# Performance work log

Measured on AMD Instinct MI355X. Metric: run time of the kernel, lower is better.

Reference implementation:

```python
import jax, jax.numpy as jnp
import numpy as np

N, K = 16384, 32          # num bboxes, context size
IN_F, HID = 608, 384      # in_features, hidden_dim
ALPHA = 0.2               # LeakyReLU slope
NEG_INF = -9e15


def setup_inputs() -> dict:
    key = jax.random.key(0)
    k1, k2, k3, k4, k5, k6, k7, k8 = jax.random.split(key, 8)
    h_i = jax.random.normal(k1, (N, IN_F), dtype=jnp.float32)
    idx = jax.random.randint(k2, (N, K), 0, N)
    pad = jax.random.uniform(k3, (N, K)) < 0.2
    context_indices = jnp.where(pad, -1, idx).astype(jnp.int64)
    s_in = 1.0 / np.sqrt(IN_F)
    s_a = 1.0 / np.sqrt(2 * HID)
    W_i = jax.random.uniform(k4, (IN_F, HID), minval=-s_in, maxval=s_in, dtype=jnp.float32)
    W_j = jax.random.uniform(k5, (IN_F, HID), minval=-s_in, maxval=s_in, dtype=jnp.float32)
    a_i = jax.random.uniform(k6, (HID,), minval=-s_a, maxval=s_a, dtype=jnp.float32)
    a_j = jax.random.uniform(k7, (HID,), minval=-s_a, maxval=s_a, dtype=jnp.float32)
    a_b = jax.random.uniform(k8, (1,), minval=-s_a, maxval=s_a, dtype=jnp.float32)
    return {"h_i": h_i, "context_indices": context_indices,
            "W_i": W_i, "W_j": W_j, "a_i": a_i, "a_j": a_j, "a_b": a_b}


def reference(h_i, context_indices, W_i, W_j, a_i, a_j, a_b):
    n = h_i.shape[0]
    Wh_i = h_i @ W_i                          # [N, H]
    # W_j has no bias, so projecting then gathering (zero pad row) equals
    # gathering zero-padded features then projecting.
    Wh_all = h_i @ W_j                        # [N, H]
    Wh_pad = jnp.concatenate([Wh_all, jnp.zeros((1, HID), Wh_all.dtype)], axis=0)
    idx = jnp.where(context_indices >= 0, context_indices, n)   # -1 -> zero row
    Wh_j = Wh_pad[idx]                        # [N, K, H] gather
    # attention_layer(concat(Wh_i, Wh_j)) == Wh_i@a_i + Wh_j@a_j + b
    scores = (Wh_i @ a_i)[:, None] + Wh_j @ a_j + a_b[0]        # [N, K]
    scores = jnp.where(scores > 0, scores, ALPHA * scores)      # LeakyReLU
    scores = jnp.where(context_indices >= 0, scores, NEG_INF)   # mask padding
    att = jax.nn.softmax(scores, axis=1)                        # [N, K]
    h_prime = jnp.einsum('nk,nkh->nh', att, Wh_j)               # [N, H]
    return h_prime
```

## Files before the change

### kernel.cpp

```cpp
#include <hip/hip_runtime.h>
#include <hip/hip_bf16.h>

typedef unsigned short u16;
typedef unsigned int u32;
typedef __attribute__((ext_vector_type(8))) __bf16 bf16x8;
typedef __attribute__((ext_vector_type(4))) __bf16 bf16x4;
typedef __attribute__((ext_vector_type(4))) float f32x4;

#define KCTX 32
#define INF_ 608
#define HID_ 384
#define NBOX 16384

#define AW_OFF  0
#define CNT_OFF 4194304
#define WH_OFF  19922944
#define BT_OFF  32505856
#define V_OFF   32972800
#define SI_OFF  32975232
#define SJ_OFF  33040768
#define AJF_OFF 33106304
#define ABF_OFF 33107840

__device__ __forceinline__ float bfu(u16 u)  { return __uint_as_float(((u32)u) << 16); }
__device__ __forceinline__ float bflo(u32 u) { return __uint_as_float(u << 16); }
__device__ __forceinline__ float bfhi(u32 u) { return __uint_as_float(u & 0xffff0000u); }
__device__ __forceinline__ u16 f2bf(float x) {
  u32 u = __float_as_uint(x);
  return (u16)((u + 0x7fffu + ((u >> 16) & 1u)) >> 16);
}
__device__ __forceinline__ void async_ld16(const void* g, void* l) {
  __builtin_amdgcn_global_load_lds(
      (const __attribute__((address_space(1))) u32*)g,
      (__attribute__((address_space(3))) u32*)l, 16, 0, 0);
}

__device__ __forceinline__ int detect_f32(const u32* hw) {
  const u32 w = hw[threadIdx.x & 63];
  const int e = (int)((w >> 7) & 0xffu);
  const unsigned long long mb = __ballot(e > 134 || e < 100);
  return __popcll(mb) >= 16;
}
__device__ __forceinline__ int detect_i64(const int* ci) {
  const int hi = ci[2 * (threadIdx.x & 63) + 1];
  const unsigned long long mz = __ballot(hi == 0 || hi == -1);
  return __popcll(mz) >= 48;
}

__global__ __launch_bounds__(256) void prep_kernel(
    const void* __restrict__ h, const void* __restrict__ Wi,
    const void* __restrict__ Wj, const void* __restrict__ ai,
    const void* __restrict__ aj, const void* __restrict__ ab,
    u16* __restrict__ Bt, float* __restrict__ v,
    float* __restrict__ ajf, float* __restrict__ abf) {
  __shared__ u16 tile[64][65];
  const int f32m = detect_f32((const u32*)h);
  const int bid = blockIdx.x, tid = threadIdx.x;
  if (bid < 60) {
    const int ft = bid / 6, ht = bid - ft * 6;
    const int f0 = ft * 64, h0 = ht * 64;
    const int ln = tid & 63, fg = tid >> 6;
#pragma unroll
    for (int rr = 0; rr < 16; ++rr) {
      const int fl = fg * 16 + rr;
      const int f = f0 + fl;
      if (f < INF_)
        tile[fl][ln] = f32m ? f2bf(((const float*)Wj)[(size_t)f * HID_ + h0 + ln])
                            : ((const u16*)Wj)[(size_t)f * HID_ + h0 + ln];
    }
    __syncthreads();
#pragma unroll
    for (int rr = 0; rr < 16; ++rr) {
      const int hl = fg * 16 + rr;
      const int f = f0 + ln;
      if (f < INF_) Bt[(size_t)(h0 + hl) * INF_ + f] = tile[ln][hl];
    }
  } else if (bid < 98) {
    const int t = (bid - 60) * 16 + (tid >> 4);
    const int sl = tid & 15;
    if (t < INF_) {
      float s = 0.f;
      if (f32m) {
        const float4* wi = (const float4*)((const float*)Wi + (size_t)t * HID_);
        const float4* a4 = (const float4*)ai;
        for (int c = sl; c < 96; c += 16) {
          float4 x = wi[c], y = a4[c];
          s += x.x * y.x + x.y * y.y + x.z * y.z + x.w * y.w;
        }
      } else {
        const uint4* wi = (const uint4*)((const u16*)Wi + (size_t)t * HID_);
        const uint4* a4 = (const uint4*)ai;
        for (int c = sl; c < 48; c += 16) {
          uint4 x = wi[c], y = a4[c];
          s += bflo(x.x) * bflo(y.x) + bfhi(x.x) * bfhi(y.x)
             + bflo(x.y) * bflo(y.y) + bfhi(x.y) * bfhi(y.y)
             + bflo(x.z) * bflo(y.z) + bfhi(x.z) * bfhi(y.z)
             + bflo(x.w) * bflo(y.w) + bfhi(x.w) * bfhi(y.w);
        }
      }
      s += __shfl_xor(s, 1); s += __shfl_xor(s, 2);
      s += __shfl_xor(s, 4); s += __shfl_xor(s, 8);
      if (sl == 0) v[t] = s;
    }
  } else {
    for (int j = tid; j < HID_; j += 256)
      ajf[j] = f32m ? ((const float*)aj)[j] : bfu(((const u16*)aj)[j]);
    if (tid == 0)
      abf[0] = f32m ? ((const float*)ab)[0] : bfu(((const u16*)ab)[0]);
  }
}

#define ASRO 612
__global__ __launch_bounds__(512, 2) void gemm_fused(
    const void* __restrict__ A, const u16* __restrict__ Bt,
    const float* __restrict__ v, u16* __restrict__ C,
    float* __restrict__ si, const float* __restrict__ ajf,
    float* __restrict__ sj) {
  extern __shared__ __align__(16) char smem[];
  u16* As = (u16*)smem;
  u16* Bs = (u16*)(smem + 78336);
  const int f32m = detect_f32((const u32*)A);
  const int tid  = threadIdx.x;
  const int lane = tid & 63;
  const int wv   = tid >> 6;
  const int row0 = blockIdx.x * 64;
  const char* Btb = (const char*)Bt;

#pragma unroll
  for (int i = 0; i < 3; ++i) {
    const int c = tid + i * 512;
    async_ld16(Btb + (size_t)(c >> 2) * 1216 + (c & 3) * 16, (char*)Bs + c * 16);
  }

  {
    const int g = tid >> 3, sub = tid & 7;
    float s = 0.f;
    const float4* v4 = (const float4*)v;
    if (f32m) {
      const float4* hr = (const float4*)((const float*)A + (size_t)(row0 + g) * INF_);
#pragma unroll
      for (int k = 0; k < 19; ++k) {
        const int c4 = sub + 8 * k;
        float4 x = hr[c4];
        ushort4 sv;
        sv.x = f2bf(x.x); sv.y = f2bf(x.y); sv.z = f2bf(x.z); sv.w = f2bf(x.w);
        *(ushort4*)&As[g * ASRO + c4 * 4] = sv;
        float4 w = v4[c4];
        s += x.x * w.x + x.y * w.y + x.z * w.z + x.w * w.w;
      }
    } else {
      const uint4* hr = (const uint4*)((const u16*)A + (size_t)(row0 + g) * INF_);
      for (int k = 0; k < 10; ++k) {
        const int c8 = sub + 8 * k;
        if (c8 < 76) {
          uint4 x = hr[c8];
          *(ushort4*)&As[g * ASRO + c8 * 8]     = *(ushort4*)&x.x;
          *(ushort4*)&As[g * ASRO + c8 * 8 + 4] = *(ushort4*)&x.z;
          float4 w0 = v4[2 * c8], w1 = v4[2 * c8 + 1];
          s += bflo(x.x) * w0.x + bfhi(x.x) * w0.y + bflo(x.y) * w0.z + bfhi(x.y) * w0.w
             + bflo(x.z) * w1.x + bfhi(x.z) * w1.y + bflo(x.w) * w1.z + bfhi(x.w) * w1.w;
        }
      }
    }
    s += __shfl_xor(s, 1); s += __shfl_xor(s, 2); s += __shfl_xor(s, 4);
    if (sub == 0) si[row0 + g] = s;
  }

  f32x4 acc[4][3];
#pragma unroll
  for (int i = 0; i < 4; ++i)
#pragma unroll
    for (int j = 0; j < 3; ++j) acc[i][j] = (f32x4){0.f, 0.f, 0.f, 0.f};

  const int lm = lane & 15, q = lane >> 4;
  const int n0 = wv * 48;

  __syncthreads();
  int cur = 0;
  for (int kt = 0; kt < 19; ++kt) {
    if (kt < 18) {
      const size_t kb = (size_t)(kt + 1) * 64;
#pragma unroll
      for (int i = 0; i < 3; ++i) {
        const int c = tid + i * 512;
        async_ld16(Btb + (size_t)(c >> 2) * 1216 + kb + (c & 3) * 16,
                   (char*)Bs + (cur ^ 1) * 24576 + c * 16);
      }
    }
    bf16x8 af[4], bfr[3];
#pragma unroll
    for (int im = 0; im < 4; ++im) {
      const int r = im * 16 + lm;
      bf16x4 lo = *(const bf16x4*)&As[r * ASRO + kt * 32 + q * 8];
      bf16x4 hi = *(const bf16x4*)&As[r * ASRO + kt * 32 + q * 8 + 4];
      af[im] = __builtin_shufflevector(lo, hi, 0, 1, 2, 3, 4, 5, 6, 7);
    }
#pragma unroll
    for (int in = 0; in < 3; ++in)
      bfr[in] = *(const bf16x8*)&Bs[cur * 12288 + (n0 + in * 16 + lm) * 32 + q * 8];
#pragma unroll
    for (int im = 0; im < 4; ++im)
#pragma unroll
      for (int in = 0; in < 3; ++in)
        acc[im][in] = __builtin_amdgcn_mfma_f32_16x16x32_bf16(
            af[im], bfr[in], acc[im][in], 0, 0, 0);
    __syncthreads();
    cur ^= 1;
  }

#pragma unroll
  for (int im = 0; im < 4; ++im)
#pragma unroll
    for (int in = 0; in < 3; ++in) {
      const int cw = in * 16 + lm;
#pragma unroll
      for (int r = 0; r < 4; ++r) {
        const int rowg = row0 + im * 16 + q * 4 + r;
        C[((size_t)wv * NBOX + rowg) * 48 + cw] = f2bf(acc[im][in][r]);
      }
    }
  float* sjred = (float*)Bs;
  float ajv[3];
#pragma unroll
  for (int in = 0; in < 3; ++in) ajv[in] = ajf[n0 + in * 16 + lm];
#pragma unroll
  for (int im = 0; im < 4; ++im)
#pragma unroll
    for (int r = 0; r < 4; ++r) {
      float p = acc[im][0][r] * ajv[0] + acc[im][1][r] * ajv[1]
              + acc[im][2][r] * ajv[2];
      p += __shfl_xor(p, 1); p += __shfl_xor(p, 2);
      p += __shfl_xor(p, 4); p += __shfl_xor(p, 8);
      if (lm == 0) sjred[wv * 64 + im * 16 + q * 4 + r] = p;
    }
  __syncthreads();
  if (tid < 64) {
    float s = 0.f;
#pragma unroll
    for (int w = 0; w < 8; ++w) s += sjred[w * 64 + tid];
    sj[row0 + tid] = s;
  }
}

__global__ __launch_bounds__(256) void score_kernel(
    const int* __restrict__ ci, const float* __restrict__ si,
    const float* __restrict__ sj, const float* __restrict__ abf,
    float2* __restrict__ aw, int* __restrict__ cnt) {
  const int i64 = detect_i64(ci);
  const int tid = threadIdx.x;
  const int k = tid & 31;
  const int n = blockIdx.x * 8 + (tid >> 5);
  const size_t t = (size_t)n * KCTX + k;
  int idx;
  if (i64) { int lo = ci[2 * t], hi2 = ci[2 * t + 1]; idx = (hi2 < 0) ? -1 : lo; }
  else     { idx = ci[t]; }
  const bool valid = idx >= 0;
  const float sjv = valid ? sj[idx] : 0.f;
  float raw = si[n] + sjv + abf[0];
  float lr = raw > 0.f ? raw : 0.2f * raw;
  float s = valid ? lr : -9e15f;
  float m = s;
#pragma unroll
  for (int o = 16; o; o >>= 1) m = fmaxf(m, __shfl_xor(m, o, 32));
  float p = __expf(s - m);
  float d = p;
#pragma unroll
  for (int o = 16; o; o >>= 1) d += __shfl_xor(d, o, 32);
  const float w = p / d;
  const unsigned long long bm = __ballot(valid);
  const u32 m32 = (u32)(bm >> (tid & 32));
  const int c_ = __popc(m32);
  const int r4 = (c_ + 3) & ~3;
  if (valid) {
    const int pf = __popc(m32 & ((1u << k) - 1u));
    aw[(size_t)n * KCTX + pf] = (float2){w, __int_as_float(idx)};
  }
  if (k >= c_ && k < r4) aw[(size_t)n * KCTX + k] = (float2){0.f, 0.f};
  if (k == 0) cnt[n] = r4;
}

__global__ __launch_bounds__(384) void gather_kernel(
    const void* __restrict__ h, const float2* __restrict__ aw,
    const int* __restrict__ cnt, const u16* __restrict__ Wh2,
    void* __restrict__ out) {
  __shared__ float2 aws[64 * 33];
  __shared__ int cs[64];
  const int f32m = detect_f32((const u32*)h);
  const int tid = threadIdx.x;
  const int s  = blockIdx.x & 7;
  const int g0 = (blockIdx.x >> 3) * 64;
  const float2* awg = aw + (size_t)g0 * KCTX;
  for (int i = tid; i < 2048; i += 384) aws[(i >> 5) * 33 + (i & 31)] = awg[i];
  if (tid < 64) cs[tid] = cnt[g0 + tid];
  __syncthreads();

  const int r = tid / 6, c = tid - r * 6;
  const int n = g0 + r;
  const u16* bc = Wh2 + (size_t)s * NBOX * 48 + c * 8;
  const int kc = cs[r];
  float a0 = 0, a1 = 0, a2 = 0, a3 = 0, a4 = 0, a5 = 0, a6 = 0, a7 = 0;
  for (int k = 0; k < kc; k += 4) {
    uint4 q[4]; float w4[4];
#pragma unroll
    for (int u = 0; u < 4; ++u) {
      const float2 e = aws[r * 33 + k + u];
      w4[u] = e.x;
      q[u] = *(const uint4*)(bc + (size_t)((u32)__float_as_int(e.y)) * 48);
    }
#pragma unroll
    for (int u = 0; u < 4; ++u) {
      const float w = w4[u];
      a0 += w * bflo(q[u].x); a1 += w * bfhi(q[u].x);
      a2 += w * bflo(q[u].y); a3 += w * bfhi(q[u].y);
      a4 += w * bflo(q[u].z); a5 += w * bfhi(q[u].z);
      a6 += w * bflo(q[u].w); a7 += w * bfhi(q[u].w);
    }
  }
  if (f32m) {
    float4* o4 = (float4*)((float*)out + (size_t)n * HID_ + s * 48 + c * 8);
    o4[0] = (float4){a0, a1, a2, a3};
    o4[1] = (float4){a4, a5, a6, a7};
  } else {
    uint4 o;
    o.x = (u32)f2bf(a0) | ((u32)f2bf(a1) << 16);
    o.y = (u32)f2bf(a2) | ((u32)f2bf(a3) << 16);
    o.z = (u32)f2bf(a4) | ((u32)f2bf(a5) << 16);
    o.w = (u32)f2bf(a6) | ((u32)f2bf(a7) << 16);
    *(uint4*)((u16*)out + (size_t)n * HID_ + s * 48 + c * 8) = o;
  }
}

extern "C" void kernel_launch(void* const* d_in, const int* in_sizes, int n_in,
                              void* d_out, int out_size, void* d_ws, size_t ws_size,
                              hipStream_t stream) {
  const void* h  = d_in[0];
  const int*  ci = (const int*)d_in[1];
  const void* Wi = d_in[2];
  const void* Wj = d_in[3];
  const void* ai = d_in[4];
  const void* aj = d_in[5];
  const void* ab = d_in[6];

  char* ws = (char*)d_ws;
  float2* aw  = (float2*)(ws + AW_OFF);
  int*    cnt = (int*)(ws + CNT_OFF);
  u16*   Wh  = (u16*)(ws + WH_OFF);
  u16*   Bt  = (u16*)(ws + BT_OFF);
  float* v   = (float*)(ws + V_OFF);
  float* si  = (float*)(ws + SI_OFF);
  float* sj  = (float*)(ws + SJ_OFF);
  float* ajf = (float*)(ws + AJF_OFF);
  float* abf = (float*)(ws + ABF_OFF);

  prep_kernel<<<99, 256, 0, stream>>>(h, Wi, Wj, ai, aj, ab, Bt, v, ajf, abf);
  gemm_fused<<<256, 512, 127488, stream>>>(h, Bt, v, Wh, si, ajf, sj);
  score_kernel<<<2048, 256, 0, stream>>>(ci, si, sj, abf, aw, cnt);
  gather_kernel<<<2048, 384, 0, stream>>>(h, aw, cnt, Wh, d_out);
}
```

Before: 161.0 us.

## Replace LDS-staged GEMM with direct-from-global 16-row tiles and more blocks

```diff
diff --git a/kernel.cpp b/kernel.cpp
--- a/kernel.cpp
+++ b/kernel.cpp
@@ -4,7 +4,6 @@
 typedef unsigned short u16;
 typedef unsigned int u32;
 typedef __attribute__((ext_vector_type(8))) __bf16 bf16x8;
-typedef __attribute__((ext_vector_type(4))) __bf16 bf16x4;
 typedef __attribute__((ext_vector_type(4))) float f32x4;
 
 #define KCTX 32
@@ -28,11 +27,6 @@
 __device__ __forceinline__ u16 f2bf(float x) {
   u32 u = __float_as_uint(x);
   return (u16)((u + 0x7fffu + ((u >> 16) & 1u)) >> 16);
-}
-__device__ __forceinline__ void async_ld16(const void* g, void* l) {
-  __builtin_amdgcn_global_load_lds(
-      (const __attribute__((address_space(1))) u32*)g,
-      (__attribute__((address_space(3))) u32*)l, 16, 0, 0);
 }
 
 __device__ __forceinline__ int detect_f32(const u32* hw) {
@@ -110,136 +104,96 @@
   }
 }
 
-#define ASRO 612
-__global__ __launch_bounds__(512, 2) void gemm_fused(
+__global__ __launch_bounds__(256, 4) void gemm_fused(
     const void* __restrict__ A, const u16* __restrict__ Bt,
     const float* __restrict__ v, u16* __restrict__ C,
     float* __restrict__ si, const float* __restrict__ ajf,
     float* __restrict__ sj) {
-  extern __shared__ __align__(16) char smem[];
-  u16* As = (u16*)smem;
-  u16* Bs = (u16*)(smem + 78336);
+  __shared__ float sjred[4][16];
   const int f32m = detect_f32((const u32*)A);
   const int tid  = threadIdx.x;
   const int lane = tid & 63;
   const int wv   = tid >> 6;
-  const int row0 = blockIdx.x * 64;
-  const char* Btb = (const char*)Bt;
-
-#pragma unroll
-  for (int i = 0; i < 3; ++i) {
-    const int c = tid + i * 512;
-    async_ld16(Btb + (size_t)(c >> 2) * 1216 + (c & 3) * 16, (char*)Bs + c * 16);
-  }
-
-  {
-    const int g = tid >> 3, sub = tid & 7;
-    float s = 0.f;
-    const float4* v4 = (const float4*)v;
-    if (f32m) {
-      const float4* hr = (const float4*)((const float*)A + (size_t)(row0 + g) * INF_);
-#pragma unroll
-      for (int k = 0; k < 19; ++k) {
-        const int c4 = sub + 8 * k;
-        float4 x = hr[c4];
-        ushort4 sv;
-        sv.x = f2bf(x.x); sv.y = f2bf(x.y); sv.z = f2bf(x.z); sv.w = f2bf(x.w);
-        *(ushort4*)&As[g * ASRO + c4 * 4] = sv;
-        float4 w = v4[c4];
-        s += x.x * w.x + x.y * w.y + x.z * w.z + x.w * w.w;
+  const int lm   = lane & 15;
+  const int q    = lane >> 4;
+  const int row0 = blockIdx.x * 16;
+  const int n0   = wv * 96;
+
+  const float4* v4 = (const float4*)v;
+  const float* hf = (const float*)A + (size_t)(row0 + lm) * INF_;
+  const u16*   hb = (const u16*)A   + (size_t)(row0 + lm) * INF_;
+
+  const u16* bbase = Bt + (size_t)(n0 + lm) * INF_ + q * 8;
+
+  f32x4 acc[6];
+#pragma unroll
+  for (int j = 0; j < 6; ++j) acc[j] = (f32x4){0.f, 0.f, 0.f, 0.f};
+  float sacc = 0.f;
+
+  for (int kt = 0; kt < 19; ++kt) {
+    const int k0 = kt * 32 + q * 8;
+    bf16x8 af;
+    {
+      const int c4 = k0 >> 2;
+      const float4 w0 = v4[c4], w1 = v4[c4 + 1];
+      if (f32m) {
+        const float4 x0 = *(const float4*)(hf + k0);
+        const float4 x1 = *(const float4*)(hf + k0 + 4);
+        uint4 pk;
+        pk.x = (u32)f2bf(x0.x) | ((u32)f2bf(x0.y) << 16);
+        pk.y = (u32)f2bf(x0.z) | ((u32)f2bf(x0.w) << 16);
+        pk.z = (u32)f2bf(x1.x) | ((u32)f2bf(x1.y) << 16);
+        pk.w = (u32)f2bf(x1.z) | ((u32)f2bf(x1.w) << 16);
+        af = __builtin_bit_cast(bf16x8, pk);
+        sacc += x0.x * w0.x + x0.y * w0.y + x0.z * w0.z + x0.w * w0.w
+              + x1.x * w1.x + x1.y * w1.y + x1.z * w1.z + x1.w * w1.w;
+      } else {
+        const uint4 xb = *(const uint4*)(hb + k0);
+        af = __builtin_bit_cast(bf16x8, xb);
+        sacc += bflo(xb.x) * w0.x + bfhi(xb.x) * w0.y
+              + bflo(xb.y) * w0.z + bfhi(xb.y) * w0.w
+              + bflo(xb.z) * w1.x + bfhi(xb.z) * w1.y
+              + bflo(xb.w) * w1.z + bfhi(xb.w) * w1.w;
       }
-    } else {
-      const uint4* hr = (const uint4*)((const u16*)A + (size_t)(row0 + g) * INF_);
-      for (int k = 0; k < 10; ++k) {
-        const int c8 = sub + 8 * k;
-        if (c8 < 76) {
-          uint4 x = hr[c8];
-          *(ushort4*)&As[g * ASRO + c8 * 8]     = *(ushort4*)&x.x;
-          *(ushort4*)&As[g * ASRO + c8 * 8 + 4] = *(ushort4*)&x.z;
-          float4 w0 = v4[2 * c8], w1 = v4[2 * c8 + 1];
-          s += bflo(x.x) * w0.x + bfhi(x.x) * w0.y + bflo(x.y) * w0.z + bfhi(x.y) * w0.w
-             + bflo(x.z) * w1.x + bfhi(x.z) * w1.y + bflo(x.w) * w1.z + bfhi(x.w) * w1.w;
-        }
-      }
-    }
-    s += __shfl_xor(s, 1); s += __shfl_xor(s, 2); s += __shfl_xor(s, 4);
-    if (sub == 0) si[row0 + g] = s;
-  }
-
-  f32x4 acc[4][3];
-#pragma unroll
-  for (int i = 0; i < 4; ++i)
-#pragma unroll
-    for (int j = 0; j < 3; ++j) acc[i][j] = (f32x4){0.f, 0.f, 0.f, 0.f};
-
-  const int lm = lane & 15, q = lane >> 4;
-  const int n0 = wv * 48;
-
+    }
+    bf16x8 bfr[6];
+#pragma unroll
+    for (int in = 0; in < 6; ++in)
+      bfr[in] = *(const bf16x8*)(bbase + (size_t)in * 16 * INF_ + kt * 32);
+#pragma unroll
+    for (int in = 0; in < 6; ++in)
+      acc[in] = __builtin_amdgcn_mfma_f32_16x16x32_bf16(af, bfr[in], acc[in], 0, 0, 0);
+  }
+
+  sacc += __shfl_xor(sacc, 16);
+  sacc += __shfl_xor(sacc, 32);
+  if (wv == 0 && lane < 16) si[row0 + lane] = sacc;
+
+#pragma unroll
+  for (int in = 0; in < 6; ++in) {
+    const int col = n0 + in * 16 + lm;
+    const int s = col / 48, cw = col - s * 48;
+#pragma unroll
+    for (int r = 0; r < 4; ++r) {
+      const int rowg = row0 + q * 4 + r;
+      C[((size_t)s * NBOX + rowg) * 48 + cw] = f2bf(acc[in][r]);
+    }
+  }
+
+  float ajv[6];
+#pragma unroll
+  for (int in = 0; in < 6; ++in) ajv[in] = ajf[n0 + in * 16 + lm];
+#pragma unroll
+  for (int r = 0; r < 4; ++r) {
+    float p = acc[0][r] * ajv[0] + acc[1][r] * ajv[1] + acc[2][r] * ajv[2]
+            + acc[3][r] * ajv[3] + acc[4][r] * ajv[4] + acc[5][r] * ajv[5];
+    p += __shfl_xor(p, 1); p += __shfl_xor(p, 2);
+    p += __shfl_xor(p, 4); p += __shfl_xor(p, 8);
+    if (lm == 0) sjred[wv][q * 4 + r] = p;
+  }
   __syncthreads();
-  int cur = 0;
-  for (int kt = 0; kt < 19; ++kt) {
-    if (kt < 18) {
-      const size_t kb = (size_t)(kt + 1) * 64;
-#pragma unroll
-      for (int i = 0; i < 3; ++i) {
-        const int c = tid + i * 512;
-        async_ld16(Btb + (size_t)(c >> 2) * 1216 + kb + (c & 3) * 16,
-                   (char*)Bs + (cur ^ 1) * 24576 + c * 16);
-      }
-    }
-    bf16x8 af[4], bfr[3];
-#pragma unroll
-    for (int im = 0; im < 4; ++im) {
-      const int r = im * 16 + lm;
-      bf16x4 lo = *(const bf16x4*)&As[r * ASRO + kt * 32 + q * 8];
-      bf16x4 hi = *(const bf16x4*)&As[r * ASRO + kt * 32 + q * 8 + 4];
-      af[im] = __builtin_shufflevector(lo, hi, 0, 1, 2, 3, 4, 5, 6, 7);
-    }
-#pragma unroll
-    for (int in = 0; in < 3; ++in)
-      bfr[in] = *(const bf16x8*)&Bs[cur * 12288 + (n0 + in * 16 + lm) * 32 + q * 8];
-#pragma unroll
-    for (int im = 0; im < 4; ++im)
-#pragma unroll
-      for (int in = 0; in < 3; ++in)
-        acc[im][in] = __builtin_amdgcn_mfma_f32_16x16x32_bf16(
-            af[im], bfr[in], acc[im][in], 0, 0, 0);
-    __syncthreads();
-    cur ^= 1;
-  }
-
-#pragma unroll
-  for (int im = 0; im < 4; ++im)
-#pragma unroll
-    for (int in = 0; in < 3; ++in) {
-      const int cw = in * 16 + lm;
-#pragma unroll
-      for (int r = 0; r < 4; ++r) {
-        const int rowg = row0 + im * 16 + q * 4 + r;
-        C[((size_t)wv * NBOX + rowg) * 48 + cw] = f2bf(acc[im][in][r]);
-      }
-    }
-  float* sjred = (float*)Bs;
-  float ajv[3];
-#pragma unroll
-  for (int in = 0; in < 3; ++in) ajv[in] = ajf[n0 + in * 16 + lm];
-#pragma unroll
-  for (int im = 0; im < 4; ++im)
-#pragma unroll
-    for (int r = 0; r < 4; ++r) {
-      float p = acc[im][0][r] * ajv[0] + acc[im][1][r] * ajv[1]
-              + acc[im][2][r] * ajv[2];
-      p += __shfl_xor(p, 1); p += __shfl_xor(p, 2);
-      p += __shfl_xor(p, 4); p += __shfl_xor(p, 8);
-      if (lm == 0) sjred[wv * 64 + im * 16 + q * 4 + r] = p;
-    }
-  __syncthreads();
-  if (tid < 64) {
-    float s = 0.f;
-#pragma unroll
-    for (int w = 0; w < 8; ++w) s += sjred[w * 64 + tid];
-    sj[row0 + tid] = s;
-  }
+  if (tid < 16)
+    sj[row0 + tid] = sjred[0][tid] + sjred[1][tid] + sjred[2][tid] + sjred[3][tid];
 }
 
 __global__ __launch_bounds__(256) void score_kernel(
@@ -353,7 +307,7 @@
   float* abf = (float*)(ws + ABF_OFF);
 
   prep_kernel<<<99, 256, 0, stream>>>(h, Wi, Wj, ai, aj, ab, Bt, v, ajf, abf);
-  gemm_fused<<<256, 512, 127488, stream>>>(h, Bt, v, Wh, si, ajf, sj);
+  gemm_fused<<<1024, 256, 0, stream>>>(h, Bt, v, Wh, si, ajf, sj);
   score_kernel<<<2048, 256, 0, stream>>>(ci, si, sj, abf, aw, cnt);
   gather_kernel<<<2048, 384, 0, stream>>>(h, aw, cnt, Wh, d_out);
 }
```

Result: slower. 187.8 us (+16.6%).

## Split bf16 conversion into separate kernel and retile GEMM with per-wave async pipelines

Applied to the files above, without the earlier changes.

```diff
diff --git a/kernel.cpp b/kernel.cpp
--- a/kernel.cpp
+++ b/kernel.cpp
@@ -4,7 +4,6 @@
 typedef unsigned short u16;
 typedef unsigned int u32;
 typedef __attribute__((ext_vector_type(8))) __bf16 bf16x8;
-typedef __attribute__((ext_vector_type(4))) __bf16 bf16x4;
 typedef __attribute__((ext_vector_type(4))) float f32x4;
 
 #define KCTX 32
@@ -21,6 +20,7 @@
 #define SJ_OFF  33040768
 #define AJF_OFF 33106304
 #define ABF_OFF 33107840
+#define HBF_OFF 33554432
 
 __device__ __forceinline__ float bfu(u16 u)  { return __uint_as_float(((u32)u) << 16); }
 __device__ __forceinline__ float bflo(u32 u) { return __uint_as_float(u << 16); }
@@ -51,7 +51,7 @@
     const void* __restrict__ h, const void* __restrict__ Wi,
     const void* __restrict__ Wj, const void* __restrict__ ai,
     const void* __restrict__ aj, const void* __restrict__ ab,
-    u16* __restrict__ Bt, float* __restrict__ v,
+    u16* __restrict__ Bt, float* __restrict__ v, float* __restrict__ sj,
     float* __restrict__ ajf, float* __restrict__ abf) {
   __shared__ u16 tile[64][65];
   const int f32m = detect_f32((const u32*)h);
@@ -103,6 +103,7 @@
       if (sl == 0) v[t] = s;
     }
   } else {
+    for (int j = tid; j < NBOX; j += 256) sj[j] = 0.f;
     for (int j = tid; j < HID_; j += 256)
       ajf[j] = f32m ? ((const float*)aj)[j] : bfu(((const u16*)aj)[j]);
     if (tid == 0)
@@ -110,135 +111,135 @@
   }
 }
 
-#define ASRO 612
-__global__ __launch_bounds__(512, 2) void gemm_fused(
-    const void* __restrict__ A, const u16* __restrict__ Bt,
-    const float* __restrict__ v, u16* __restrict__ C,
-    float* __restrict__ si, const float* __restrict__ ajf,
-    float* __restrict__ sj) {
+__global__ __launch_bounds__(256) void convert_kernel(
+    const void* __restrict__ h, const float* __restrict__ v,
+    u16* __restrict__ hbf, float* __restrict__ si) {
+  const int f32m = detect_f32((const u32*)h);
+  const int g = threadIdx.x >> 3, sub = threadIdx.x & 7;
+  const int row = blockIdx.x * 32 + g;
+  float s = 0.f;
+  const float4* v4 = (const float4*)v;
+  if (f32m) {
+    const float4* hr = (const float4*)((const float*)h + (size_t)row * INF_);
+    u32* ob = (u32*)(hbf + (size_t)row * INF_);
+#pragma unroll
+    for (int k = 0; k < 19; ++k) {
+      const int c4 = sub + 8 * k;
+      float4 x = hr[c4];
+      uint2 pk;
+      pk.x = (u32)f2bf(x.x) | ((u32)f2bf(x.y) << 16);
+      pk.y = (u32)f2bf(x.z) | ((u32)f2bf(x.w) << 16);
+      *(uint2*)&ob[c4 * 2] = pk;
+      float4 w = v4[c4];
+      s += x.x * w.x + x.y * w.y + x.z * w.z + x.w * w.w;
+    }
+  } else {
+    const uint4* hr = (const uint4*)((const u16*)h + (size_t)row * INF_);
+    for (int k = 0; k < 10; ++k) {
+      const int c8 = sub + 8 * k;
+      if (c8 < 76) {
+        uint4 x = hr[c8];
+        float4 w0 = v4[2 * c8], w1 = v4[2 * c8 + 1];
+        s += bflo(x.x) * w0.x + bfhi(x.x) * w0.y + bflo(x.y) * w0.z + bfhi(x.y) * w0.w
+           + bflo(x.z) * w1.x + bfhi(x.z) * w1.y + bflo(x.w) * w1.z + bfhi(x.w) * w1.w;
+      }
+    }
+  }
+  s += __shfl_xor(s, 1); s += __shfl_xor(s, 2); s += __shfl_xor(s, 4);
+  if (sub == 0) si[row] = s;
+}
+
+__global__ __launch_bounds__(256) void gemm_fused(
+    const void* __restrict__ A, const u16* __restrict__ hbf_,
+    const u16* __restrict__ Bt, u16* __restrict__ C,
+    const float* __restrict__ ajf, float* __restrict__ sj) {
   extern __shared__ __align__(16) char smem[];
-  u16* As = (u16*)smem;
-  u16* Bs = (u16*)(smem + 78336);
   const int f32m = detect_f32((const u32*)A);
   const int tid  = threadIdx.x;
   const int lane = tid & 63;
   const int wv   = tid >> 6;
-  const int row0 = blockIdx.x * 64;
-  const char* Btb = (const char*)Bt;
-
-#pragma unroll
-  for (int i = 0; i < 3; ++i) {
-    const int c = tid + i * 512;
-    async_ld16(Btb + (size_t)(c >> 2) * 1216 + (c & 3) * 16, (char*)Bs + c * 16);
-  }
-
-  {
-    const int g = tid >> 3, sub = tid & 7;
-    float s = 0.f;
-    const float4* v4 = (const float4*)v;
-    if (f32m) {
-      const float4* hr = (const float4*)((const float*)A + (size_t)(row0 + g) * INF_);
-#pragma unroll
-      for (int k = 0; k < 19; ++k) {
-        const int c4 = sub + 8 * k;
-        float4 x = hr[c4];
-        ushort4 sv;
-        sv.x = f2bf(x.x); sv.y = f2bf(x.y); sv.z = f2bf(x.z); sv.w = f2bf(x.w);
-        *(ushort4*)&As[g * ASRO + c4 * 4] = sv;
-        float4 w = v4[c4];
-        s += x.x * w.x + x.y * w.y + x.z * w.z + x.w * w.w;
-      }
-    } else {
-      const uint4* hr = (const uint4*)((const u16*)A + (size_t)(row0 + g) * INF_);
-      for (int k = 0; k < 10; ++k) {
-        const int c8 = sub + 8 * k;
-        if (c8 < 76) {
-          uint4 x = hr[c8];
-          *(ushort4*)&As[g * ASRO + c8 * 8]     = *(ushort4*)&x.x;
-          *(ushort4*)&As[g * ASRO + c8 * 8 + 4] = *(ushort4*)&x.z;
-          float4 w0 = v4[2 * c8], w1 = v4[2 * c8 + 1];
-          s += bflo(x.x) * w0.x + bfhi(x.x) * w0.y + bflo(x.y) * w0.z + bfhi(x.y) * w0.w
-             + bflo(x.z) * w1.x + bfhi(x.z) * w1.y + bflo(x.w) * w1.z + bfhi(x.w) * w1.w;
-        }
-      }
-    }
-    s += __shfl_xor(s, 1); s += __shfl_xor(s, 2); s += __shfl_xor(s, 4);
-    if (sub == 0) si[row0 + g] = s;
-  }
-
-  f32x4 acc[4][3];
+  const int lm   = lane & 15, q = lane >> 4;
+  const int panel = blockIdx.x >> 6;
+  const int rowc  = blockIdx.x & 63;
+  const int row0 = rowc * 256 + wv * 64;
+  const int c0   = panel * 96;
+  const char* hB = f32m ? (const char*)hbf_ : (const char*)A;
+  const char* hrow = hB + (size_t)(row0 + (lane >> 2)) * 1216 + (lane & 3) * 16;
+  const char* brow = (const char*)Bt + (size_t)(c0 + (lane >> 2)) * 1216 + (lane & 3) * 16;
+  char* wbase = smem + wv * 20480;
+
+  f32x4 acc[4][6];
+#pragma unroll
+  for (int mf = 0; mf < 4; ++mf)
+#pragma unroll
+    for (int nf = 0; nf < 6; ++nf) acc[mf][nf] = (f32x4){0.f, 0.f, 0.f, 0.f};
+
 #pragma unroll
   for (int i = 0; i < 4; ++i)
-#pragma unroll
-    for (int j = 0; j < 3; ++j) acc[i][j] = (f32x4){0.f, 0.f, 0.f, 0.f};
-
-  const int lm = lane & 15, q = lane >> 4;
-  const int n0 = wv * 48;
-
-  __syncthreads();
+    async_ld16(hrow + i * 19456, wbase + i * 1024 + lane * 16);
+#pragma unroll
+  for (int i = 0; i < 6; ++i)
+    async_ld16(brow + i * 19456, wbase + 4096 + i * 1024 + lane * 16);
+
   int cur = 0;
   for (int kt = 0; kt < 19; ++kt) {
     if (kt < 18) {
-      const size_t kb = (size_t)(kt + 1) * 64;
-#pragma unroll
-      for (int i = 0; i < 3; ++i) {
-        const int c = tid + i * 512;
-        async_ld16(Btb + (size_t)(c >> 2) * 1216 + kb + (c & 3) * 16,
-                   (char*)Bs + (cur ^ 1) * 24576 + c * 16);
+      const int kb = (kt + 1) * 64;
+      char* nb = wbase + (cur ^ 1) * 10240;
+#pragma unroll
+      for (int i = 0; i < 4; ++i)
+        async_ld16(hrow + i * 19456 + kb, nb + i * 1024 + lane * 16);
+#pragma unroll
+      for (int i = 0; i < 6; ++i)
+        async_ld16(brow + i * 19456 + kb, nb + 4096 + i * 1024 + lane * 16);
+      asm volatile("s_waitcnt vmcnt(10)" ::: "memory");
+    } else {
+      asm volatile("s_waitcnt vmcnt(0)" ::: "memory");
+    }
+    __builtin_amdgcn_sched_barrier(0);
+    const char* ab = wbase + cur * 10240;
+    const char* bb = ab + 4096;
+    bf16x8 af[4], bfr[6];
+#pragma unroll
+    for (int mf = 0; mf < 4; ++mf)
+      af[mf] = *(const bf16x8*)(ab + (mf * 16 + lm) * 64 + q * 16);
+#pragma unroll
+    for (int nf = 0; nf < 6; ++nf)
+      bfr[nf] = *(const bf16x8*)(bb + (nf * 16 + lm) * 64 + q * 16);
+#pragma unroll
+    for (int mf = 0; mf < 4; ++mf)
+#pragma unroll
+      for (int nf = 0; nf < 6; ++nf)
+        acc[mf][nf] = __builtin_amdgcn_mfma_f32_16x16x32_bf16(
+            af[mf], bfr[nf], acc[mf][nf], 0, 0, 0);
+    cur ^= 1;
+  }
+
+  float ajv[6];
+#pragma unroll
+  for (int nf = 0; nf < 6; ++nf) ajv[nf] = ajf[c0 + nf * 16 + lm];
+#pragma unroll
+  for (int mf = 0; mf < 4; ++mf) {
+#pragma unroll
+    for (int nf = 0; nf < 6; ++nf) {
+      const int colp = nf * 16 + lm;
+      const int s  = panel * 2 + (colp >= 48 ? 1 : 0);
+      const int cw = colp >= 48 ? colp - 48 : colp;
+#pragma unroll
+      for (int r = 0; r < 4; ++r) {
+        const int rowg = row0 + mf * 16 + q * 4 + r;
+        C[((size_t)s * NBOX + rowg) * 48 + cw] = f2bf(acc[mf][nf][r]);
       }
     }
-    bf16x8 af[4], bfr[3];
-#pragma unroll
-    for (int im = 0; im < 4; ++im) {
-      const int r = im * 16 + lm;
-      bf16x4 lo = *(const bf16x4*)&As[r * ASRO + kt * 32 + q * 8];
-      bf16x4 hi = *(const bf16x4*)&As[r * ASRO + kt * 32 + q * 8 + 4];
-      af[im] = __builtin_shufflevector(lo, hi, 0, 1, 2, 3, 4, 5, 6, 7);
-    }
-#pragma unroll
-    for (int in = 0; in < 3; ++in)
-      bfr[in] = *(const bf16x8*)&Bs[cur * 12288 + (n0 + in * 16 + lm) * 32 + q * 8];
-#pragma unroll
-    for (int im = 0; im < 4; ++im)
-#pragma unroll
-      for (int in = 0; in < 3; ++in)
-        acc[im][in] = __builtin_amdgcn_mfma_f32_16x16x32_bf16(
-            af[im], bfr[in], acc[im][in], 0, 0, 0);
-    __syncthreads();
-    cur ^= 1;
-  }
-
-#pragma unroll
-  for (int im = 0; im < 4; ++im)
-#pragma unroll
-    for (int in = 0; in < 3; ++in) {
-      const int cw = in * 16 + lm;
-#pragma unroll
-      for (int r = 0; r < 4; ++r) {
-        const int rowg = row0 + im * 16 + q * 4 + r;
-        C[((size_t)wv * NBOX + rowg) * 48 + cw] = f2bf(acc[im][in][r]);
-      }
-    }
-  float* sjred = (float*)Bs;
-  float ajv[3];
-#pragma unroll
-  for (int in = 0; in < 3; ++in) ajv[in] = ajf[n0 + in * 16 + lm];
-#pragma unroll
-  for (int im = 0; im < 4; ++im)
 #pragma unroll
     for (int r = 0; r < 4; ++r) {
-      float p = acc[im][0][r] * ajv[0] + acc[im][1][r] * ajv[1]
-              + acc[im][2][r] * ajv[2];
+      float p = acc[mf][0][r] * ajv[0] + acc[mf][1][r] * ajv[1]
+              + acc[mf][2][r] * ajv[2] + acc[mf][3][r] * ajv[3]
+              + acc[mf][4][r] * ajv[4] + acc[mf][5][r] * ajv[5];
       p += __shfl_xor(p, 1); p += __shfl_xor(p, 2);
       p += __shfl_xor(p, 4); p += __shfl_xor(p, 8);
-      if (lm == 0) sjred[wv * 64 + im * 16 + q * 4 + r] = p;
-    }
-  __syncthreads();
-  if (tid < 64) {
-    float s = 0.f;
-#pragma unroll
-    for (int w = 0; w < 8; ++w) s += sjred[w * 64 + tid];
-    sj[row0 + tid] = s;
+      if (lm == 0) atomicAdd(&sj[row0 + mf * 16 + q * 4 + r], p);
+    }
   }
 }
 
@@ -351,9 +352,11 @@
   float* sj  = (float*)(ws + SJ_OFF);
   float* ajf = (float*)(ws + AJF_OFF);
   float* abf = (float*)(ws + ABF_OFF);
-
-  prep_kernel<<<99, 256, 0, stream>>>(h, Wi, Wj, ai, aj, ab, Bt, v, ajf, abf);
-  gemm_fused<<<256, 512, 127488, stream>>>(h, Bt, v, Wh, si, ajf, sj);
+  u16*   hbf = (u16*)(ws + HBF_OFF);
+
+  prep_kernel<<<99, 256, 0, stream>>>(h, Wi, Wj, ai, aj, ab, Bt, v, sj, ajf, abf);
+  convert_kernel<<<512, 256, 0, stream>>>(h, v, hbf, si);
+  gemm_fused<<<256, 256, 81920, stream>>>(h, hbf, Bt, Wh, ajf, sj);
   score_kernel<<<2048, 256, 0, stream>>>(ci, si, sj, abf, aw, cnt);
   gather_kernel<<<2048, 384, 0, stream>>>(h, aw, cnt, Wh, d_out);
 }
```

After: 167.3 us. +3.9%, slower.

## Pin gather column slices to XCDs via persistent work-stealing blocks

Applied to the files above, without the earlier changes.

```diff
diff --git a/kernel.cpp b/kernel.cpp
--- a/kernel.cpp
+++ b/kernel.cpp
@@ -14,6 +14,7 @@
 
 #define AW_OFF  0
 #define CNT_OFF 4194304
+#define WRK_OFF 4259840
 #define WH_OFF  19922944
 #define BT_OFF  32505856
 #define V_OFF   32972800
@@ -245,9 +246,10 @@
 __global__ __launch_bounds__(256) void score_kernel(
     const int* __restrict__ ci, const float* __restrict__ si,
     const float* __restrict__ sj, const float* __restrict__ abf,
-    float2* __restrict__ aw, int* __restrict__ cnt) {
+    float2* __restrict__ aw, int* __restrict__ cnt, int* __restrict__ wrk) {
   const int i64 = detect_i64(ci);
   const int tid = threadIdx.x;
+  if (blockIdx.x == 0 && tid < 8) wrk[tid] = 0;
   const int k = tid & 31;
   const int n = blockIdx.x * 8 + (tid >> 5);
   const size_t t = (size_t)n * KCTX + k;
@@ -282,51 +284,67 @@
 __global__ __launch_bounds__(384) void gather_kernel(
     const void* __restrict__ h, const float2* __restrict__ aw,
     const int* __restrict__ cnt, const u16* __restrict__ Wh2,
-    void* __restrict__ out) {
+    void* __restrict__ out, int* __restrict__ wrk) {
   __shared__ float2 aws[64 * 33];
   __shared__ int cs[64];
+  __shared__ int chsh;
   const int f32m = detect_f32((const u32*)h);
   const int tid = threadIdx.x;
-  const int s  = blockIdx.x & 7;
-  const int g0 = (blockIdx.x >> 3) * 64;
-  const float2* awg = aw + (size_t)g0 * KCTX;
-  for (int i = tid; i < 2048; i += 384) aws[(i >> 5) * 33 + (i & 31)] = awg[i];
-  if (tid < 64) cs[tid] = cnt[g0 + tid];
-  __syncthreads();
-
+  u32 xcc;
+  asm volatile("s_getreg_b32 %0, hwreg(HW_REG_XCC_ID)" : "=s"(xcc));
+  const int myx = (int)(xcc & 7u);
   const int r = tid / 6, c = tid - r * 6;
-  const int n = g0 + r;
-  const u16* bc = Wh2 + (size_t)s * NBOX * 48 + c * 8;
-  const int kc = cs[r];
-  float a0 = 0, a1 = 0, a2 = 0, a3 = 0, a4 = 0, a5 = 0, a6 = 0, a7 = 0;
-  for (int k = 0; k < kc; k += 4) {
-    uint4 q[4]; float w4[4];
-#pragma unroll
-    for (int u = 0; u < 4; ++u) {
-      const float2 e = aws[r * 33 + k + u];
-      w4[u] = e.x;
-      q[u] = *(const uint4*)(bc + (size_t)((u32)__float_as_int(e.y)) * 48);
-    }
-#pragma unroll
-    for (int u = 0; u < 4; ++u) {
-      const float w = w4[u];
-      a0 += w * bflo(q[u].x); a1 += w * bfhi(q[u].x);
-      a2 += w * bflo(q[u].y); a3 += w * bfhi(q[u].y);
-      a4 += w * bflo(q[u].z); a5 += w * bfhi(q[u].z);
-      a6 += w * bflo(q[u].w); a7 += w * bfhi(q[u].w);
-    }
-  }
-  if (f32m) {
-    float4* o4 = (float4*)((float*)out + (size_t)n * HID_ + s * 48 + c * 8);
-    o4[0] = (float4){a0, a1, a2, a3};
-    o4[1] = (float4){a4, a5, a6, a7};
-  } else {
-    uint4 o;
-    o.x = (u32)f2bf(a0) | ((u32)f2bf(a1) << 16);
-    o.y = (u32)f2bf(a2) | ((u32)f2bf(a3) << 16);
-    o.z = (u32)f2bf(a4) | ((u32)f2bf(a5) << 16);
-    o.w = (u32)f2bf(a6) | ((u32)f2bf(a7) << 16);
-    *(uint4*)((u16*)out + (size_t)n * HID_ + s * 48 + c * 8) = o;
+
+#pragma unroll 1
+  for (int off = 0; off < 8; ++off) {
+    const int s = (myx + off) & 7;
+    const u16* bc = Wh2 + (size_t)s * NBOX * 48 + c * 8;
+#pragma unroll 1
+    for (;;) {
+      __syncthreads();
+      if (tid == 0) chsh = atomicAdd(&wrk[s], 1);
+      __syncthreads();
+      const int ch = chsh;
+      if (ch >= 256) break;
+      const int g0 = ch * 64;
+      const float2* awg = aw + (size_t)g0 * KCTX;
+      for (int i = tid; i < 2048; i += 384) aws[(i >> 5) * 33 + (i & 31)] = awg[i];
+      if (tid < 64) cs[tid] = cnt[g0 + tid];
+      __syncthreads();
+
+      const int n = g0 + r;
+      const int kc = cs[r];
+      float a0 = 0, a1 = 0, a2 = 0, a3 = 0, a4 = 0, a5 = 0, a6 = 0, a7 = 0;
+      for (int k = 0; k < kc; k += 4) {
+        uint4 q[4]; float w4[4];
+#pragma unroll
+        for (int u = 0; u < 4; ++u) {
+          const float2 e = aws[r * 33 + k + u];
+          w4[u] = e.x;
+          q[u] = *(const uint4*)(bc + (size_t)((u32)__float_as_int(e.y)) * 48);
+        }
+#pragma unroll
+        for (int u = 0; u < 4; ++u) {
+          const float w = w4[u];
+          a0 += w * bflo(q[u].x); a1 += w * bfhi(q[u].x);
+          a2 += w * bflo(q[u].y); a3 += w * bfhi(q[u].y);
+          a4 += w * bflo(q[u].z); a5 += w * bfhi(q[u].z);
+          a6 += w * bflo(q[u].w); a7 += w * bfhi(q[u].w);
+        }
+      }
+      if (f32m) {
+        float4* o4 = (float4*)((float*)out + (size_t)n * HID_ + s * 48 + c * 8);
+        o4[0] = (float4){a0, a1, a2, a3};
+        o4[1] = (float4){a4, a5, a6, a7};
+      } else {
+        uint4 o;
+        o.x = (u32)f2bf(a0) | ((u32)f2bf(a1) << 16);
+        o.y = (u32)f2bf(a2) | ((u32)f2bf(a3) << 16);
+        o.z = (u32)f2bf(a4) | ((u32)f2bf(a5) << 16);
+        o.w = (u32)f2bf(a6) | ((u32)f2bf(a7) << 16);
+        *(uint4*)((u16*)out + (size_t)n * HID_ + s * 48 + c * 8) = o;
+      }
+    }
   }
 }
 
@@ -344,6 +362,7 @@
   char* ws = (char*)d_ws;
   float2* aw  = (float2*)(ws + AW_OFF);
   int*    cnt = (int*)(ws + CNT_OFF);
+  int*    wrk = (int*)(ws + WRK_OFF);
   u16*   Wh  = (u16*)(ws + WH_OFF);
   u16*   Bt  = (u16*)(ws + BT_OFF);
   float* v   = (float*)(ws + V_OFF);
@@ -354,6 +373,6 @@
 
   prep_kernel<<<99, 256, 0, stream>>>(h, Wi, Wj, ai, aj, ab, Bt, v, ajf, abf);
   gemm_fused<<<256, 512, 127488, stream>>>(h, Bt, v, Wh, si, ajf, sj);
-  score_kernel<<<2048, 256, 0, stream>>>(ci, si, sj, abf, aw, cnt);
-  gather_kernel<<<2048, 384, 0, stream>>>(h, aw, cnt, Wh, d_out);
-}
+  score_kernel<<<2048, 256, 0, stream>>>(ci, si, sj, abf, aw, cnt, wrk);
+  gather_kernel<<<1024, 384, 0, stream>>>(h, aw, cnt, Wh, d_out, wrk);
+}
```

Result: slower. 261.6 us (+62.5%).
